# Optimization experiments

Hardware: AMD Instinct MI355X
Metric: run time of the kernel (lower is better)

The kernel has to match this reference:

```python
import jax, jax.numpy as jnp
import numpy as np

H = 4096      # hidden_size
NH = 32       # num heads
HD = H // NH  # head_dim = 128
I = 11008     # intermediate_size
T = 1024      # prompt tokens
G = 128       # AWQ group size
EPS = 1e-6
ROPE_BASE = 10000.0


def _pack4(key, in_f, out_f):
    # pack 8 uint4 nibbles per int32, [in_f, out_f/8]
    nib = jax.random.randint(key, (in_f, out_f // 8, 8), 0, 16, dtype=jnp.int32)
    shifts = (jnp.arange(8, dtype=jnp.int32) * 4)
    return jnp.bitwise_or.reduce(nib << shifts, axis=-1).astype(jnp.int32)


def _dequant(qw, qz, sc):
    # qw:[in,out/8] int32, qz:[in/G,out/8] int32, sc:[in/G,out] float
    shifts = jnp.arange(8, dtype=jnp.int32) * 4
    w = ((qw[:, :, None] >> shifts) & 0xF).reshape(qw.shape[0], -1)   # [in,out]
    z = ((qz[:, :, None] >> shifts) & 0xF).reshape(qz.shape[0], -1)   # [groups,out]
    gidx = jnp.arange(qw.shape[0]) // G
    return (w.astype(sc.dtype) - z.astype(sc.dtype)[gidx]) * sc[gidx]


def _qlinear(x, qw, qz, sc):
    return x @ _dequant(qw, qz, sc)


def _rmsnorm(x, w):
    var = jnp.mean(x * x, axis=-1, keepdims=True)
    return x * jax.lax.rsqrt(var + EPS) * w


def _rope(x, positions):
    # x: [T, NH, HD], neox-style half rotation (vLLM rotary)
    inv = 1.0 / (ROPE_BASE ** (jnp.arange(0, HD, 2, dtype=jnp.float32) / HD))
    freqs = positions.astype(jnp.float32)[:, None] * inv[None, :]     # [T, HD/2]
    cos = jnp.cos(freqs)[:, None, :]
    sin = jnp.sin(freqs)[:, None, :]
    x1, x2 = jnp.split(x, 2, axis=-1)
    return jnp.concatenate([x1 * cos - x2 * sin, x2 * cos + x1 * sin], axis=-1)


def _attention(positions, q, k, v):
    # causal self-attention over the prompt (prefill writes k/v to cache then attends)
    q = _rope(q.reshape(T, NH, HD), positions)
    k = _rope(k.reshape(T, NH, HD), positions)
    v = v.reshape(T, NH, HD)
    scale = HD ** -0.5
    scores = jnp.einsum('qhd,khd->hqk', q, k) * scale
    mask = jnp.tril(jnp.ones((T, T), dtype=bool))
    scores = jnp.where(mask[None], scores, jnp.finfo(scores.dtype).min)
    probs = jax.nn.softmax(scores, axis=-1)
    out = jnp.einsum('hqk,khd->qhd', probs, v)
    return out.reshape(T, NH * HD)


def setup_inputs() -> dict:
    key = jax.random.key(0)
    ks = jax.random.split(key, 16)
    S = 0.002  # AWQ scale magnitude
    inp = {
        'positions': jnp.arange(T, dtype=jnp.int32),
        'hidden_states': jax.random.normal(ks[0], (T, H), dtype=jnp.float32),
        'ln1_w': jnp.ones((H,), dtype=jnp.float32),
        'ln2_w': jnp.ones((H,), dtype=jnp.float32),
        'qkv_qw': _pack4(ks[1], H, 3 * H),
        'qkv_qz': _pack4(ks[2], H // G, 3 * H),
        'qkv_sc': jax.random.uniform(ks[3], (H // G, 3 * H), dtype=jnp.float32) * S,
        'o_qw': _pack4(ks[4], H, H),
        'o_qz': _pack4(ks[5], H // G, H),
        'o_sc': jax.random.uniform(ks[6], (H // G, H), dtype=jnp.float32) * S,
        'gate_qw': _pack4(ks[7], H, I),
        'gate_qz': _pack4(ks[8], H // G, I),
        'gate_sc': jax.random.uniform(ks[9], (H // G, I), dtype=jnp.float32) * S,
        'up_qw': _pack4(ks[10], H, I),
        'up_qz': _pack4(ks[11], H // G, I),
        'up_sc': jax.random.uniform(ks[12], (H // G, I), dtype=jnp.float32) * S,
        'down_qw': _pack4(ks[13], I, H),
        'down_qz': _pack4(ks[14], I // G, H),
        'down_sc': jax.random.uniform(ks[15], (I // G, H), dtype=jnp.float32) * S,
    }
    return inp


def reference(positions, hidden_states, ln1_w, qkv_qw, qkv_qz, qkv_sc,
              o_qw, o_qz, o_sc, gate_qw, gate_qz, gate_sc,
              up_qw, up_qz, up_sc, down_qw, down_qz, down_sc, ln2_w):
    # --- self attention block ---
    residual = hidden_states
    x = _rmsnorm(hidden_states, ln1_w)
    qkv = _qlinear(x, qkv_qw, qkv_qz, qkv_sc)                # [T, 3H]
    q, k, v = jnp.split(qkv, 3, axis=-1)
    attn_out = _attention(positions, q, k, v)                # [T, H]
    x = _qlinear(attn_out, o_qw, o_qz, o_sc)
    hidden = residual + x
    # --- MLP block ---
    residual = hidden
    x = _rmsnorm(hidden, ln2_w)
    gate = jax.nn.silu(_qlinear(x, gate_qw, gate_qz, gate_sc))
    up = _qlinear(x, up_qw, up_qz, up_sc)
    x = _qlinear(gate * up, down_qw, down_qz, down_sc)
    return residual + x
```

## Files before the change

kernel.cpp:

```cpp
#include <hip/hip_runtime.h>
#include <cstdint>

typedef __attribute__((ext_vector_type(8))) short  bf16x8;
typedef __attribute__((ext_vector_type(4))) float  f32x4;
typedef __attribute__((ext_vector_type(4))) unsigned int uint4v;
typedef __attribute__((ext_vector_type(2))) unsigned int uint2v;

typedef const __attribute__((address_space(1))) void* gas_t;
typedef __attribute__((address_space(3))) void* las_t;

__device__ __forceinline__ float bf2f(unsigned short b) {
    union { unsigned int u; float f; } v; v.u = ((unsigned int)b) << 16; return v.f;
}
__device__ __forceinline__ unsigned short f2bf(float f) {
    union { float f; unsigned int u; } v; v.f = f;
    unsigned int r = v.u + 0x7FFFu + ((v.u >> 16) & 1u);
    return (unsigned short)(r >> 16);
}
__device__ __forceinline__ float u2f(unsigned int u) {
    union { unsigned int u; float f; } v; v.u = u; return v.f;
}

__device__ __forceinline__ void dequant_block(int bx, int by, int t,
    const int* __restrict__ qw, const int* __restrict__ qz,
    const float* __restrict__ sc, unsigned short* __restrict__ out,
    int NW, int K)
{
    const int wcb = bx << 5;
    const int kb  = by << 6;
    const int g   = by >> 1;
    const int N   = NW << 3;
    const int wc  = wcb + (t >> 3);
    const int k0  = kb + ((t & 7) << 3);

    unsigned int w[8];
#pragma unroll
    for (int j = 0; j < 8; j++) w[j] = (unsigned int)qw[(size_t)(k0 + j) * NW + wc];
    const unsigned int zw = (unsigned int)qz[(size_t)g * NW + wc];
    float scv[8];
#pragma unroll
    for (int j2 = 0; j2 < 8; j2++) scv[j2] = sc[(size_t)g * N + (wc << 3) + j2];

#pragma unroll
    for (int j2 = 0; j2 < 8; j2++) {
        const int sh = j2 << 2;
        const float s = scv[j2];
        const float moff = -(8388608.0f + (float)((zw >> sh) & 0xFu)) * s;
        unsigned int pk[4];
#pragma unroll
        for (int i = 0; i < 4; i++) {
            float f0 = fmaf(u2f(((w[2*i]   >> sh) & 0xFu) | 0x4B000000u), s, moff);
            float f1 = fmaf(u2f(((w[2*i+1] >> sh) & 0xFu) | 0x4B000000u), s, moff);
            asm("v_cvt_pk_bf16_f32 %0, %1, %2" : "=v"(pk[i]) : "v"(f0), "v"(f1));
        }
        uint4v ov = {pk[0], pk[1], pk[2], pk[3]};
        *(uint4v*)(out + (size_t)((wc << 3) + j2) * K + k0) = ov;
    }
}

__global__ __launch_bounds__(256)
void dequant_kernel(const int* __restrict__ qw, const int* __restrict__ qz,
                    const float* __restrict__ sc, unsigned short* __restrict__ out,
                    int NW, int K)
{
    dequant_block(blockIdx.x, blockIdx.y, threadIdx.x, qw, qz, sc, out, NW, K);
}

__global__ __launch_bounds__(256)
void rmsnorm_kernel(const float* __restrict__ x, const float* __restrict__ wgt,
                    unsigned short* __restrict__ out)
{
    const int t = blockIdx.x, tid = threadIdx.x;
    const float4* xr = (const float4*)(x + (size_t)t * 4096);
    float4 v[4];
    float ss = 0.f;
#pragma unroll
    for (int j = 0; j < 4; j++) {
        v[j] = xr[(j << 8) + tid];
        ss += v[j].x*v[j].x + v[j].y*v[j].y + v[j].z*v[j].z + v[j].w*v[j].w;
    }
#pragma unroll
    for (int m = 1; m < 64; m <<= 1) ss += __shfl_xor(ss, m);
    __shared__ float red[4];
    if ((tid & 63) == 0) red[tid >> 6] = ss;
    __syncthreads();
    float tot = red[0] + red[1] + red[2] + red[3];
    float rs = rsqrtf(tot * (1.f / 4096.f) + 1e-6f);
    const float4* wr = (const float4*)wgt;
#pragma unroll
    for (int j = 0; j < 4; j++) {
        float4 wv = wr[(j << 8) + tid];
        float4 xv = v[j];
        unsigned int p0 = (unsigned int)f2bf(xv.x*rs*wv.x) | ((unsigned int)f2bf(xv.y*rs*wv.y) << 16);
        unsigned int p1 = (unsigned int)f2bf(xv.z*rs*wv.z) | ((unsigned int)f2bf(xv.w*rs*wv.w) << 16);
        uint2v pk = {p0, p1};
        *(uint2v*)(&out[(size_t)t*4096 + (size_t)(((j << 8) + tid) << 2)]) = pk;
    }
}

template<int MODE>
__global__ __launch_bounds__(256, 4)
void bt_gemm(const unsigned short* __restrict__ A,
             const unsigned short* __restrict__ Bt0,
             const unsigned short* __restrict__ Bt1,
             void* __restrict__ out0, void* __restrict__ out1,
             const float* __restrict__ res,
             int N, int K, int NB, int gemmBlocks, int ksplit,
             const int* dq1_qw, const int* dq1_qz, const float* dq1_sc,
             unsigned short* dq1_out, int dq1_NW, int dq1_K, int dq1_blocks,
             const int* dq2_qw, const int* dq2_qz, const float* dq2_sc,
             unsigned short* dq2_out, int dq2_NW, int dq2_K)
{
    const int flat = blockIdx.x;
    if (flat >= gemmBlocks) {
        if (blockIdx.z != 0) return;
        int db = flat - gemmBlocks;
        if (db < dq1_blocks) {
            int xb = dq1_NW >> 5;
            dequant_block(db % xb, db / xb, threadIdx.x, dq1_qw, dq1_qz, dq1_sc, dq1_out, dq1_NW, dq1_K);
        } else {
            db -= dq1_blocks;
            int xb = dq2_NW >> 5;
            dequant_block(db % xb, db / xb, threadIdx.x, dq2_qw, dq2_qz, dq2_sc, dq2_out, dq2_NW, dq2_K);
        }
        return;
    }

    const int work = NB * (flat & 7) + (flat >> 3);
    const int n0 = (work >> 3) << 7;
    const int m0 = (work & 7) << 7;
    const int z  = blockIdx.z;

    const unsigned short* Bt = Bt0;
    void* outp = out0;
    if (MODE == 1 && z == 1) { Bt = Bt1; outp = out1; }
    const int k0base = (MODE == 2) ? z * ksplit : 0;
    const int nsteps = ((MODE == 2) ? ksplit : K) >> 6;

    __shared__ unsigned short As[128 * 64];
    __shared__ unsigned short Bs[128 * 64];

    const int tid  = threadIdx.x;
    const int lane = tid & 63;
    const int wid  = tid >> 6;
    const int wm   = wid >> 1, wn = wid & 1;

    f32x4 acc[4][4];
#pragma unroll
    for (int i = 0; i < 4; i++)
#pragma unroll
        for (int j = 0; j < 4; j++) { f32x4 zv = {0.f,0.f,0.f,0.f}; acc[i][j] = zv; }

    for (int t = 0; t < nsteps; t++) {
        const int k0 = k0base + (t << 6);
        __syncthreads();
#pragma unroll
        for (int i = 0; i < 4; i++) {
            int slot = (i << 8) + tid;
            int row = slot >> 3, s = slot & 7;
            __builtin_amdgcn_global_load_lds(
                (gas_t)(A + (size_t)(m0 + row) * K + k0 + ((s ^ (row & 7)) << 3)),
                (las_t)&As[slot << 3], 16, 0, 0);
        }
#pragma unroll
        for (int i = 0; i < 4; i++) {
            int slot = (i << 8) + tid;
            int row = slot >> 3, s = slot & 7;
            __builtin_amdgcn_global_load_lds(
                (gas_t)(Bt + (size_t)(n0 + row) * K + k0 + ((s ^ (row & 7)) << 3)),
                (las_t)&Bs[slot << 3], 16, 0, 0);
        }
        __syncthreads();
#pragma unroll
        for (int kk = 0; kk < 2; kk++) {
            const int srow = (kk << 2) + (lane >> 4);
            bf16x8 af[4], bfv[4];
#pragma unroll
            for (int mi = 0; mi < 4; mi++) {
                int r = (wm << 6) + (mi << 4) + (lane & 15);
                af[mi] = *(const bf16x8*)(&As[(r << 6) + ((srow ^ (r & 7)) << 3)]);
            }
#pragma unroll
            for (int ni = 0; ni < 4; ni++) {
                int r = (wn << 6) + (ni << 4) + (lane & 15);
                bfv[ni] = *(const bf16x8*)(&Bs[(r << 6) + ((srow ^ (r & 7)) << 3)]);
            }
#pragma unroll
            for (int mi = 0; mi < 4; mi++)
#pragma unroll
                for (int ni = 0; ni < 4; ni++)
                    acc[mi][ni] = __builtin_amdgcn_mfma_f32_16x16x32_bf16(af[mi], bfv[ni], acc[mi][ni], 0, 0, 0);
        }
    }

    const int rbase = m0 + (wm << 6) + ((lane >> 4) << 2);
    const int cbase = n0 + (wn << 6) + (lane & 15);
#pragma unroll
    for (int mi = 0; mi < 4; mi++) {
#pragma unroll
        for (int r = 0; r < 4; r++) {
            int row = rbase + (mi << 4) + r;
#pragma unroll
            for (int ni = 0; ni < 4; ni++) {
                int col = cbase + (ni << 4);
                float v = acc[mi][ni][r];
                if (MODE == 3) {
                    ((float*)out0)[(size_t)row * N + col] = v + res[(size_t)row * N + col];
                } else if (MODE == 2) {
                    ((unsigned short*)out0)[(size_t)z * ((size_t)1024 * N) + (size_t)row * N + col] = f2bf(v);
                } else {
                    ((unsigned short*)outp)[(size_t)row * N + col] = f2bf(v);
                }
            }
        }
    }
}

__global__ __launch_bounds__(256)
void reduce2_kernel(const float* __restrict__ base, const unsigned short* __restrict__ part,
                    float* __restrict__ out)
{
    const size_t i = (size_t)blockIdx.x * 256 + threadIdx.x;
    const size_t stride = (size_t)1024 * 4096;
    float s[8];
    float4 a0 = ((const float4*)base)[2*i], a1 = ((const float4*)base)[2*i+1];
    s[0]=a0.x; s[1]=a0.y; s[2]=a0.z; s[3]=a0.w; s[4]=a1.x; s[5]=a1.y; s[6]=a1.z; s[7]=a1.w;
#pragma unroll
    for (int p = 0; p < 2; p++) {
        uint4v v = *(const uint4v*)(part + p * stride + i * 8);
#pragma unroll
        for (int j = 0; j < 4; j++) {
            s[2*j]   += bf2f((unsigned short)(v[j] & 0xFFFF));
            s[2*j+1] += bf2f((unsigned short)(v[j] >> 16));
        }
    }
    float4 o0 = {s[0],s[1],s[2],s[3]}, o1 = {s[4],s[5],s[6],s[7]};
    ((float4*)out)[2*i] = o0; ((float4*)out)[2*i+1] = o1;
}

__global__ __launch_bounds__(256)
void rope_kernel(const int* __restrict__ positions, const unsigned short* __restrict__ qkv,
                 unsigned short* __restrict__ Qr, unsigned short* __restrict__ Kr,
                 unsigned short* __restrict__ Vtp)
{
    const int t = blockIdx.x, tid = threadIdx.x;
    const float p = (float)positions[t];
    const unsigned short* row = qkv + (size_t)t * 12288;
#pragma unroll 4
    for (int it = 0; it < 16; it++) {
        int task = (it << 8) + tid;
        int i   = task & 63;
        int hh  = (task >> 6) & 31;
        int isK = task >> 11;
        float fr = p * __expf(-(float)i * 0.14391156831f);
        float s, c;
        __sincosf(fr, &s, &c);
        const unsigned short* src = row + (isK << 12) + (hh << 7);
        float x1 = bf2f(src[i]);
        float x2 = bf2f(src[64 + i]);
        float o1 = x1 * c - x2 * s;
        float o2 = x2 * c + x1 * s;
        if (!isK) { o1 *= 0.08838834764831845f; o2 *= 0.08838834764831845f; }
        unsigned short* dst = (isK ? Kr : Qr) + ((size_t)hh * 1024 + t) * 128;
        dst[i]      = f2bf(o1);
        dst[64 + i] = f2bf(o2);
    }
#pragma unroll 4
    for (int it = 0; it < 16; it++) {
        int task = (it << 8) + tid;
        int d = task & 127, hh = task >> 7;
        Vtp[((size_t)hh * 128 + d) * 1024 + t] = row[8192 + task];
    }
}

__global__ __launch_bounds__(256, 2)
void attn_kernel(const unsigned short* __restrict__ Qr, const unsigned short* __restrict__ Kr,
                 const unsigned short* __restrict__ Vtp, unsigned short* __restrict__ attn_out)
{
    __shared__ unsigned short Ks[64 * 128];
    __shared__ unsigned short Vs[128 * 64];
    __shared__ unsigned short Ps[4][16 * 64];
    const int tid = threadIdx.x, lane = tid & 63, w = tid >> 6;
    const int qt = blockIdx.x, h = blockIdx.y;

    const unsigned short* Qh = Qr + ((size_t)h * 1024 + (size_t)qt * 64) * 128;

    bf16x8 qf[4];
#pragma unroll
    for (int kk = 0; kk < 4; kk++)
        qf[kk] = *(const bf16x8*)(Qh + (size_t)((w << 4) + (lane & 15)) * 128 + (kk << 5) + ((lane >> 4) << 3));

    f32x4 o[8];
#pragma unroll
    for (int i = 0; i < 8; i++) { f32x4 zf = {0.f,0.f,0.f,0.f}; o[i] = zf; }
    float Mr[4] = {-1e30f, -1e30f, -1e30f, -1e30f};
    float Lr[4] = {0.f, 0.f, 0.f, 0.f};
    const int qrow0 = (qt << 6) + (w << 4) + ((lane >> 4) << 2);

    for (int kt = 0; kt <= qt; kt++) {
        __syncthreads();
#pragma unroll
        for (int j = 0; j < 4; j++) {
            int slot = (j << 8) + tid;
            int rw = slot >> 4, s = slot & 15;
            int ssrc = (s & 8) | ((s ^ (rw & 7)) & 7);
            const uint4v* src = (const uint4v*)(Kr + ((size_t)h * 1024 + (size_t)kt * 64 + rw) * 128 + (ssrc << 3));
            *(uint4v*)(&Ks[(rw << 7) + (s << 3)]) = *src;
        }
#pragma unroll
        for (int j = 0; j < 4; j++) {
            int slot = (j << 8) + tid;
            int rw = slot >> 3, s = slot & 7;
            const uint4v* src = (const uint4v*)(Vtp + ((size_t)h * 128 + rw) * 1024 + (kt << 6) + ((s ^ (rw & 7)) << 3));
            *(uint4v*)(&Vs[(rw << 6) + (s << 3)]) = *src;
        }
        __syncthreads();

        f32x4 sc4[4];
#pragma unroll
        for (int ni = 0; ni < 4; ni++) { f32x4 zf = {0.f,0.f,0.f,0.f}; sc4[ni] = zf; }
#pragma unroll
        for (int kk = 0; kk < 4; kk++) {
#pragma unroll
            for (int ni = 0; ni < 4; ni++) {
                int r = (ni << 4) + (lane & 15);
                int s = (kk << 2) + (lane >> 4);
                int sp = (s & 8) | ((s ^ (r & 7)) & 7);
                bf16x8 kf = *(const bf16x8*)(&Ks[(r << 7) + (sp << 3)]);
                sc4[ni] = __builtin_amdgcn_mfma_f32_16x16x32_bf16(qf[kk], kf, sc4[ni], 0, 0, 0);
            }
        }

#pragma unroll
        for (int r = 0; r < 4; r++) {
            int qg = qrow0 + r;
            float mx = -1e30f;
#pragma unroll
            for (int ni = 0; ni < 4; ni++) {
                int kg_ = (kt << 6) + (ni << 4) + (lane & 15);
                float v = sc4[ni][r];
                if (kt == qt && kg_ > qg) { v = -1e30f; sc4[ni][r] = v; }
                mx = fmaxf(mx, v);
            }
#pragma unroll
            for (int m_ = 1; m_ < 16; m_ <<= 1) mx = fmaxf(mx, __shfl_xor(mx, m_));
            float mnew  = fmaxf(Mr[r], mx);
            float alpha = __expf(Mr[r] - mnew);
            Mr[r] = mnew;
            float rs = 0.f;
#pragma unroll
            for (int ni = 0; ni < 4; ni++) {
                float pv = __expf(sc4[ni][r] - mnew);
                sc4[ni][r] = pv;
                rs += pv;
            }
#pragma unroll
            for (int m_ = 1; m_ < 16; m_ <<= 1) rs += __shfl_xor(rs, m_);
            Lr[r] = Lr[r] * alpha + rs;
#pragma unroll
            for (int nd = 0; nd < 8; nd++) o[nd][r] *= alpha;
        }

#pragma unroll
        for (int r = 0; r < 4; r++) {
            int qr = ((lane >> 4) << 2) + r;
#pragma unroll
            for (int ni = 0; ni < 4; ni++) {
                int col = (ni << 4) + (lane & 15);
                int phys = (col >> 3) ^ (qr & 7);
                Ps[w][(qr << 6) + (phys << 3) + (col & 7)] = f2bf(sc4[ni][r]);
            }
        }
#pragma unroll
        for (int kk2 = 0; kk2 < 2; kk2++) {
            int rowp = lane & 15;
            int sl = (kk2 << 2) + (lane >> 4);
            bf16x8 pa = *(const bf16x8*)(&Ps[w][(rowp << 6) + ((sl ^ (rowp & 7)) << 3)]);
#pragma unroll
            for (int nd = 0; nd < 8; nd++) {
                int rv = (nd << 4) + (lane & 15);
                bf16x8 vb = *(const bf16x8*)(&Vs[(rv << 6) + ((sl ^ (rv & 7)) << 3)]);
                o[nd] = __builtin_amdgcn_mfma_f32_16x16x32_bf16(pa, vb, o[nd], 0, 0, 0);
            }
        }
    }

#pragma unroll
    for (int r = 0; r < 4; r++) {
        float inv = 1.0f / Lr[r];
        int trow = qrow0 + r;
#pragma unroll
        for (int nd = 0; nd < 8; nd++) {
            int col = (h << 7) + (nd << 4) + (lane & 15);
            attn_out[(size_t)trow * 4096 + col] = f2bf(o[nd][r] * inv);
        }
    }
}

__global__ __launch_bounds__(256)
void silu_deq_kernel(const unsigned short* __restrict__ gate, unsigned short* __restrict__ up,
                     int siluBlocks,
                     const int* __restrict__ qw, const int* __restrict__ qz,
                     const float* __restrict__ sc, unsigned short* __restrict__ wout,
                     int NW, int K)
{
    if (blockIdx.x >= siluBlocks) {
        int db = blockIdx.x - siluBlocks;
        int xb = NW >> 5;
        dequant_block(db % xb, db / xb, threadIdx.x, qw, qz, sc, wout, NW, K);
        return;
    }
    size_t idx = ((size_t)blockIdx.x * 256 + threadIdx.x) * 8;
    uint4v g = *(const uint4v*)(gate + idx);
    uint4v u = *(const uint4v*)(up + idx);
    unsigned int outp[4];
#pragma unroll
    for (int j = 0; j < 4; j++) {
        unsigned int gw = g[j], uw = u[j];
        float g0 = bf2f((unsigned short)(gw & 0xFFFF)), g1 = bf2f((unsigned short)(gw >> 16));
        float u0 = bf2f((unsigned short)(uw & 0xFFFF)), u1 = bf2f((unsigned short)(uw >> 16));
        float s0 = g0 / (1.f + __expf(-g0)) * u0;
        float s1 = g1 / (1.f + __expf(-g1)) * u1;
        outp[j] = (unsigned int)f2bf(s0) | ((unsigned int)f2bf(s1) << 16);
    }
    uint4v ov = {outp[0], outp[1], outp[2], outp[3]};
    *(uint4v*)(up + idx) = ov;
}

extern "C" void kernel_launch(void* const* d_in, const int* in_sizes, int n_in,
                              void* d_out, int out_size, void* d_ws, size_t ws_size,
                              hipStream_t stream)
{
    const int*   positions = (const int*)  d_in[0];
    const float* hidden    = (const float*)d_in[1];
    const float* ln1       = (const float*)d_in[2];
    const float* ln2       = (const float*)d_in[3];
    const int*   qkv_qw    = (const int*)  d_in[4];
    const int*   qkv_qz    = (const int*)  d_in[5];
    const float* qkv_sc    = (const float*)d_in[6];
    const int*   o_qw      = (const int*)  d_in[7];
    const int*   o_qz      = (const int*)  d_in[8];
    const float* o_sc      = (const float*)d_in[9];
    const int*   gate_qw   = (const int*)  d_in[10];
    const int*   gate_qz   = (const int*)  d_in[11];
    const float* gate_sc   = (const float*)d_in[12];
    const int*   up_qw     = (const int*)  d_in[13];
    const int*   up_qz     = (const int*)  d_in[14];
    const float* up_sc     = (const float*)d_in[15];
    const int*   down_qw   = (const int*)  d_in[16];
    const int*   down_qz   = (const int*)  d_in[17];
    const float* down_sc   = (const float*)d_in[18];

    char* ws = (char*)d_ws;
    const size_t MB = 1 << 20;
    unsigned short* W_qkv = (unsigned short*)(ws + 0);
    unsigned short* Qrp   = (unsigned short*)(ws + 0);
    unsigned short* Krp   = (unsigned short*)(ws + 8 * MB);
    unsigned short* Vtp   = (unsigned short*)(ws + 16 * MB);
    unsigned short* W_gate= (unsigned short*)(ws + 0);
    unsigned short* W_down= (unsigned short*)(ws + 0);
    unsigned short* attnb = (unsigned short*)(ws + 86 * MB);
    unsigned short* W_o   = (unsigned short*)(ws + 96 * MB);
    unsigned short* gateb = (unsigned short*)(ws + 96 * MB);
    unsigned short* part  = (unsigned short*)(ws + 96 * MB);
    unsigned short* W_up  = (unsigned short*)(ws + 128 * MB);
    unsigned short* xln   = (unsigned short*)(ws + 214 * MB);
    unsigned short* qkvb  = (unsigned short*)(ws + 222 * MB);
    unsigned short* upb   = (unsigned short*)(ws + 222 * MB);
    float*          hid   = (float*)d_out;

    dequant_kernel<<<dim3(48, 64), 256, 0, stream>>>(qkv_qw, qkv_qz, qkv_sc, W_qkv, 1536, 4096);
    rmsnorm_kernel<<<1024, 256, 0, stream>>>(hidden, ln1, xln);
    bt_gemm<0><<<768 + 1024 + 2752, 256, 0, stream>>>(
        xln, W_qkv, nullptr, (void*)qkvb, nullptr, nullptr,
        12288, 4096, 96, 768, 0,
        o_qw, o_qz, o_sc, W_o, 512, 4096, 1024,
        up_qw, up_qz, up_sc, W_up, 1376, 4096);
    rope_kernel<<<1024, 256, 0, stream>>>(positions, qkvb, Qrp, Krp, Vtp);
    attn_kernel<<<dim3(16, 32), 256, 0, stream>>>(Qrp, Krp, Vtp, attnb);
    bt_gemm<3><<<256 + 2752, 256, 0, stream>>>(
        attnb, W_o, nullptr, (void*)hid, nullptr, hidden,
        4096, 4096, 32, 256, 0,
        gate_qw, gate_qz, gate_sc, W_gate, 1376, 4096, 2752,
        nullptr, nullptr, nullptr, nullptr, 32, 64);
    rmsnorm_kernel<<<1024, 256, 0, stream>>>(hid, ln2, xln);
    bt_gemm<1><<<dim3(688, 1, 2), 256, 0, stream>>>(
        xln, W_gate, W_up, (void*)gateb, (void*)upb, nullptr,
        11008, 4096, 86, 688, 0,
        nullptr, nullptr, nullptr, nullptr, 32, 64, 0,
        nullptr, nullptr, nullptr, nullptr, 32, 64);
    silu_deq_kernel<<<5504 + 2752, 256, 0, stream>>>(
        gateb, upb, 5504, down_qw, down_qz, down_sc, W_down, 512, 11008);
    bt_gemm<2><<<dim3(256, 1, 2), 256, 0, stream>>>(
        upb, W_down, nullptr, (void*)part, nullptr, nullptr,
        4096, 11008, 32, 256, 5504,
        nullptr, nullptr, nullptr, nullptr, 32, 64, 0,
        nullptr, nullptr, nullptr, nullptr, 32, 64);
    reduce2_kernel<<<2048, 256, 0, stream>>>(hid, part, (float*)d_out);
}
```

Before: 685.8 us.

## Co-schedule dequant with rmsnorm and attention, split down GEMM four ways

Fuses the QKV weight dequant with the first RMSNorm into one launch. Moves the up-projection dequant out of the QKV GEMM launch and into the attention launch as extra blocks, so that dequant work fills idle CUs while attention runs. The down-projection K-split goes from 2 to 4 partitions, with a matching 4-way reduce, to raise parallelism. The cost is more partial-sum traffic in bf16 and a larger part buffer, which could overlap other workspace regions, along with extra blocks competing with attention for CUs.

```diff
diff --git a/kernel.cpp b/kernel.cpp
--- a/kernel.cpp
+++ b/kernel.cpp
@@ -59,11 +59,44 @@
 }
 
 __global__ __launch_bounds__(256)
-void dequant_kernel(const int* __restrict__ qw, const int* __restrict__ qz,
-                    const float* __restrict__ sc, unsigned short* __restrict__ out,
-                    int NW, int K)
-{
-    dequant_block(blockIdx.x, blockIdx.y, threadIdx.x, qw, qz, sc, out, NW, K);
+void deq_rms_kernel(const int* __restrict__ qw, const int* __restrict__ qz,
+                    const float* __restrict__ sc, unsigned short* __restrict__ wout,
+                    int NW, int K, int deqBlocks,
+                    const float* __restrict__ x, const float* __restrict__ lnw,
+                    unsigned short* __restrict__ xout)
+{
+    __shared__ float red[4];
+    const int tid = threadIdx.x;
+    if (blockIdx.x < (unsigned)deqBlocks) {
+        int xb = NW >> 5;
+        dequant_block(blockIdx.x % xb, blockIdx.x / xb, tid, qw, qz, sc, wout, NW, K);
+        return;
+    }
+    const int t = blockIdx.x - deqBlocks;
+    const float4* xr = (const float4*)(x + (size_t)t * 4096);
+    float4 v[4];
+    float ss = 0.f;
+#pragma unroll
+    for (int j = 0; j < 4; j++) {
+        v[j] = xr[(j << 8) + tid];
+        ss += v[j].x*v[j].x + v[j].y*v[j].y + v[j].z*v[j].z + v[j].w*v[j].w;
+    }
+#pragma unroll
+    for (int m = 1; m < 64; m <<= 1) ss += __shfl_xor(ss, m);
+    if ((tid & 63) == 0) red[tid >> 6] = ss;
+    __syncthreads();
+    float tot = red[0] + red[1] + red[2] + red[3];
+    float rs = rsqrtf(tot * (1.f / 4096.f) + 1e-6f);
+    const float4* wr = (const float4*)lnw;
+#pragma unroll
+    for (int j = 0; j < 4; j++) {
+        float4 wv = wr[(j << 8) + tid];
+        float4 xv = v[j];
+        unsigned int p0 = (unsigned int)f2bf(xv.x*rs*wv.x) | ((unsigned int)f2bf(xv.y*rs*wv.y) << 16);
+        unsigned int p1 = (unsigned int)f2bf(xv.z*rs*wv.z) | ((unsigned int)f2bf(xv.w*rs*wv.w) << 16);
+        uint2v pk = {p0, p1};
+        *(uint2v*)(&xout[(size_t)t*4096 + (size_t)(((j << 8) + tid) << 2)]) = pk;
+    }
 }
 
 __global__ __launch_bounds__(256)
@@ -107,22 +140,14 @@
              const float* __restrict__ res,
              int N, int K, int NB, int gemmBlocks, int ksplit,
              const int* dq1_qw, const int* dq1_qz, const float* dq1_sc,
-             unsigned short* dq1_out, int dq1_NW, int dq1_K, int dq1_blocks,
-             const int* dq2_qw, const int* dq2_qz, const float* dq2_sc,
-             unsigned short* dq2_out, int dq2_NW, int dq2_K)
+             unsigned short* dq1_out, int dq1_NW, int dq1_K)
 {
     const int flat = blockIdx.x;
     if (flat >= gemmBlocks) {
         if (blockIdx.z != 0) return;
         int db = flat - gemmBlocks;
-        if (db < dq1_blocks) {
-            int xb = dq1_NW >> 5;
-            dequant_block(db % xb, db / xb, threadIdx.x, dq1_qw, dq1_qz, dq1_sc, dq1_out, dq1_NW, dq1_K);
-        } else {
-            db -= dq1_blocks;
-            int xb = dq2_NW >> 5;
-            dequant_block(db % xb, db / xb, threadIdx.x, dq2_qw, dq2_qz, dq2_sc, dq2_out, dq2_NW, dq2_K);
-        }
+        int xb = dq1_NW >> 5;
+        dequant_block(db % xb, db / xb, threadIdx.x, dq1_qw, dq1_qz, dq1_sc, dq1_out, dq1_NW, dq1_K);
         return;
     }
 
@@ -217,7 +242,7 @@
 }
 
 __global__ __launch_bounds__(256)
-void reduce2_kernel(const float* __restrict__ base, const unsigned short* __restrict__ part,
+void reduce4_kernel(const float* __restrict__ base, const unsigned short* __restrict__ part,
                     float* __restrict__ out)
 {
     const size_t i = (size_t)blockIdx.x * 256 + threadIdx.x;
@@ -226,7 +251,7 @@
     float4 a0 = ((const float4*)base)[2*i], a1 = ((const float4*)base)[2*i+1];
     s[0]=a0.x; s[1]=a0.y; s[2]=a0.z; s[3]=a0.w; s[4]=a1.x; s[5]=a1.y; s[6]=a1.z; s[7]=a1.w;
 #pragma unroll
-    for (int p = 0; p < 2; p++) {
+    for (int p = 0; p < 4; p++) {
         uint4v v = *(const uint4v*)(part + p * stride + i * 8);
 #pragma unroll
         for (int j = 0; j < 4; j++) {
@@ -275,13 +300,23 @@
 
 __global__ __launch_bounds__(256, 2)
 void attn_kernel(const unsigned short* __restrict__ Qr, const unsigned short* __restrict__ Kr,
-                 const unsigned short* __restrict__ Vtp, unsigned short* __restrict__ attn_out)
-{
+                 const unsigned short* __restrict__ Vtp, unsigned short* __restrict__ attn_out,
+                 int attnBlocks,
+                 const int* __restrict__ dqw, const int* __restrict__ dqz,
+                 const float* __restrict__ dsc, unsigned short* __restrict__ dwout,
+                 int dNW, int dK)
+{
+    if (blockIdx.x >= (unsigned)attnBlocks) {
+        int db = blockIdx.x - attnBlocks;
+        int xb = dNW >> 5;
+        dequant_block(db % xb, db / xb, threadIdx.x, dqw, dqz, dsc, dwout, dNW, dK);
+        return;
+    }
     __shared__ unsigned short Ks[64 * 128];
     __shared__ unsigned short Vs[128 * 64];
     __shared__ unsigned short Ps[4][16 * 64];
     const int tid = threadIdx.x, lane = tid & 63, w = tid >> 6;
-    const int qt = blockIdx.x, h = blockIdx.y;
+    const int qt = blockIdx.x & 15, h = blockIdx.x >> 4;
 
     const unsigned short* Qh = Qr + ((size_t)h * 1024 + (size_t)qt * 64) * 128;
 
@@ -404,7 +439,7 @@
                      const float* __restrict__ sc, unsigned short* __restrict__ wout,
                      int NW, int K)
 {
-    if (blockIdx.x >= siluBlocks) {
+    if (blockIdx.x >= (unsigned)siluBlocks) {
         int db = blockIdx.x - siluBlocks;
         int xb = NW >> 5;
         dequant_block(db % xb, db / xb, threadIdx.x, qw, qz, sc, wout, NW, K);
@@ -469,32 +504,31 @@
     unsigned short* upb   = (unsigned short*)(ws + 222 * MB);
     float*          hid   = (float*)d_out;
 
-    dequant_kernel<<<dim3(48, 64), 256, 0, stream>>>(qkv_qw, qkv_qz, qkv_sc, W_qkv, 1536, 4096);
-    rmsnorm_kernel<<<1024, 256, 0, stream>>>(hidden, ln1, xln);
-    bt_gemm<0><<<768 + 1024 + 2752, 256, 0, stream>>>(
+    deq_rms_kernel<<<3072 + 1024, 256, 0, stream>>>(
+        qkv_qw, qkv_qz, qkv_sc, W_qkv, 1536, 4096, 3072,
+        hidden, ln1, xln);
+    bt_gemm<0><<<768 + 1024, 256, 0, stream>>>(
         xln, W_qkv, nullptr, (void*)qkvb, nullptr, nullptr,
         12288, 4096, 96, 768, 0,
-        o_qw, o_qz, o_sc, W_o, 512, 4096, 1024,
+        o_qw, o_qz, o_sc, W_o, 512, 4096);
+    rope_kernel<<<1024, 256, 0, stream>>>(positions, qkvb, Qrp, Krp, Vtp);
+    attn_kernel<<<512 + 2752, 256, 0, stream>>>(
+        Qrp, Krp, Vtp, attnb, 512,
         up_qw, up_qz, up_sc, W_up, 1376, 4096);
-    rope_kernel<<<1024, 256, 0, stream>>>(positions, qkvb, Qrp, Krp, Vtp);
-    attn_kernel<<<dim3(16, 32), 256, 0, stream>>>(Qrp, Krp, Vtp, attnb);
     bt_gemm<3><<<256 + 2752, 256, 0, stream>>>(
         attnb, W_o, nullptr, (void*)hid, nullptr, hidden,
         4096, 4096, 32, 256, 0,
-        gate_qw, gate_qz, gate_sc, W_gate, 1376, 4096, 2752,
-        nullptr, nullptr, nullptr, nullptr, 32, 64);
+        gate_qw, gate_qz, gate_sc, W_gate, 1376, 4096);
     rmsnorm_kernel<<<1024, 256, 0, stream>>>(hid, ln2, xln);
     bt_gemm<1><<<dim3(688, 1, 2), 256, 0, stream>>>(
         xln, W_gate, W_up, (void*)gateb, (void*)upb, nullptr,
         11008, 4096, 86, 688, 0,
-        nullptr, nullptr, nullptr, nullptr, 32, 64, 0,
         nullptr, nullptr, nullptr, nullptr, 32, 64);
     silu_deq_kernel<<<5504 + 2752, 256, 0, stream>>>(
         gateb, upb, 5504, down_qw, down_qz, down_sc, W_down, 512, 11008);
-    bt_gemm<2><<<dim3(256, 1, 2), 256, 0, stream>>>(
+    bt_gemm<2><<<dim3(256, 1, 4), 256, 0, stream>>>(
         upb, W_down, nullptr, (void*)part, nullptr, nullptr,
-        4096, 11008, 32, 256, 5504,
-        nullptr, nullptr, nullptr, nullptr, 32, 64, 0,
+        4096, 11008, 32, 256, 2752,
         nullptr, nullptr, nullptr, nullptr, 32, 64);
-    reduce2_kernel<<<2048, 256, 0, stream>>>(hid, part, (float*)d_out);
-}
+    reduce4_kernel<<<2048, 256, 0, stream>>>(hid, part, (float*)d_out);
+}
```

Result: no change. 680.4 us (median of 2 runs) (-0.8%).
